# Kernel optimization log

Hardware: AMD Instinct MI355X
Metric: run time of the kernel (lower is better)

Reference implementation:

```python
import jax, jax.numpy as jnp
import numpy as np

BLOCK = 32          # MXFP block size (OCP microscaling)
EMAX_FP4 = 2.0      # max exponent of FP4 E2M1 (max value 6.0 = 1.5 * 2^2)
FP4_MAX = 6.0       # saturation value of E2M1
E8M0_MIN, E8M0_MAX = -127.0, 127.0


def _quant_dequant_mxfp(t, block_dim):
    """Fake-quantize tensor t to MXFP4 (E2M1 elements, shared E8M0 scale per
    block of 32 along block_dim), then dequantize back to float."""
    t = jnp.moveaxis(t, block_dim, -1)
    shape = t.shape
    nb = shape[-1] // BLOCK
    tb = t.reshape(shape[:-1] + (nb, BLOCK))

    # shared power-of-two scale from block absmax: scale = 2^(floor(log2 amax) - emax)
    amax = jnp.max(jnp.abs(tb), axis=-1, keepdims=True)
    safe_amax = jnp.where(amax > 0, amax, 1.0)
    shared_exp = jnp.floor(jnp.log2(safe_amax)) - EMAX_FP4
    scale = jnp.exp2(jnp.clip(shared_exp, E8M0_MIN, E8M0_MAX))

    v = tb / scale
    sign = jnp.sign(v)
    a = jnp.clip(jnp.abs(v), 0.0, FP4_MAX)  # saturate to E2M1 max
    # E2M1 quantization step: 0.5 for |v|<2 (incl. subnormals), 1 for [2,4), 2 for [4,6]
    e = jnp.clip(jnp.floor(jnp.log2(jnp.maximum(a, 2.0 ** -10))), 0.0, EMAX_FP4)
    step = jnp.exp2(e - 1.0)
    q = jnp.round(a / step) * step

    deq = (sign * q * scale).reshape(shape)
    return jnp.moveaxis(deq, -1, block_dim)


def setup_inputs() -> dict:
    key = jax.random.key(0)
    kx, kw, kb = jax.random.split(key, 3)
    x = jax.random.normal(kx, (64, 4096), dtype=jnp.float32)
    weight = jax.random.normal(kw, (11008, 4096), dtype=jnp.float32) * 0.02
    bias = jax.random.normal(kb, (11008,), dtype=jnp.float32) * 0.02
    return {"x": x, "weight": weight, "bias": bias}


def reference(x, weight, bias):
    # layer_type = 'XqWqBq': MXFP4 quant-dequant on x (last dim), w (in_features
    # dim, block_dim=1) and b (dim 0), fused with the linear GEMM.
    x_dq = _quant_dequant_mxfp(x, block_dim=-1)        # [T, Din]
    w_dq = _quant_dequant_mxfp(weight, block_dim=1)    # [Dout, Din]
    b_dq = _quant_dequant_mxfp(bias, block_dim=0)      # [Dout]
    return jnp.einsum('ti,oi->to', x_dq, w_dq) + b_dq  # [T, Dout]
```

## Files before the change

### kernel.cpp

```cpp
#include <hip/hip_runtime.h>
#include <hip/hip_bf16.h>

#define DIN   4096
#define DOUT  11008
#define TM    64
#define KSPLIT 4
#define KCHUNK (DIN / KSPLIT)

typedef __attribute__((ext_vector_type(8))) short  bf16x8;
typedef __attribute__((ext_vector_type(4))) float  f32x4;

__device__ inline void mx_block_scale(float amax, float& scale, float& inv_scale) {
    float safe = amax > 0.0f ? amax : 1.0f;
    int e = (int)((__float_as_uint(safe) >> 23) & 255) - 127;
    int se = e - 2;
    if (se < -127) se = -127;
    scale     = ldexpf(1.0f, se);
    inv_scale = ldexpf(1.0f, -se);
}

__device__ inline float mx_qd(float v, float scale, float inv_scale) {
    float a = fabsf(v) * inv_scale;
    a = fminf(a, 6.0f);
    float step, rstep;
    if (a < 2.0f)      { step = 0.5f; rstep = 2.0f; }
    else if (a < 4.0f) { step = 1.0f; rstep = 1.0f; }
    else               { step = 2.0f; rstep = 0.5f; }
    float q = rintf(a * rstep) * step;
    return copysignf(q * scale, v);
}

__device__ inline unsigned short f32_to_bf16_bits(float f) {
    return (unsigned short)(__float_as_uint(f) >> 16);
}

__global__ __launch_bounds__(256) void quant_x_kernel(const float* __restrict__ x,
                                                      unsigned short* __restrict__ x_dq) {
    int gid = blockIdx.x * 256 + threadIdx.x;
    const float4 v = *(const float4*)(x + (size_t)gid * 4);
    float am = fmaxf(fmaxf(fabsf(v.x), fabsf(v.y)), fmaxf(fabsf(v.z), fabsf(v.w)));
    am = fmaxf(am, __shfl_xor(am, 1));
    am = fmaxf(am, __shfl_xor(am, 2));
    am = fmaxf(am, __shfl_xor(am, 4));
    float scale, inv;
    mx_block_scale(am, scale, inv);
    ushort4 q;
    q.x = f32_to_bf16_bits(mx_qd(v.x, scale, inv));
    q.y = f32_to_bf16_bits(mx_qd(v.y, scale, inv));
    q.z = f32_to_bf16_bits(mx_qd(v.z, scale, inv));
    q.w = f32_to_bf16_bits(mx_qd(v.w, scale, inv));
    *(ushort4*)(x_dq + (size_t)gid * 4) = q;
}

__global__ __launch_bounds__(64) void init_out_kernel(const float* __restrict__ bias,
                                                      float* __restrict__ out) {
    int n = blockIdx.x * 64 + threadIdx.x;
    float v = bias[n];
    float am = fabsf(v);
    am = fmaxf(am, __shfl_xor(am, 1));
    am = fmaxf(am, __shfl_xor(am, 2));
    am = fmaxf(am, __shfl_xor(am, 4));
    am = fmaxf(am, __shfl_xor(am, 8));
    am = fmaxf(am, __shfl_xor(am, 16));
    float scale, inv;
    mx_block_scale(am, scale, inv);
    float b = mx_qd(v, scale, inv);
    for (int t = 0; t < TM; ++t)
        out[(size_t)t * DOUT + n] = b;
}

__global__ __launch_bounds__(256) void gemm_kernel(const unsigned short* __restrict__ x_dq,
                                                   const float* __restrict__ wgt,
                                                   float* __restrict__ out) {
    __shared__ unsigned short x_lds[TM * 32];
    __shared__ unsigned short w_lds[32 * 32];

    const int t     = threadIdx.x;
    const int lane  = t & 63;
    const int wid   = t >> 6;
    const int n0    = blockIdx.x * 32;
    const int kbase = blockIdx.y * KCHUNK;

    const int wrow = t >> 3;
    const int wcol = (t & 7) * 4;
    const int xrow = t >> 2;
    const int xcol = (t & 3) * 8;

    const float*          wptr = wgt + (size_t)(n0 + wrow) * DIN + kbase + wcol;
    const unsigned short* xptr = x_dq + (size_t)xrow * DIN + kbase + xcol;

    const int a_off  = (wid * 16 + (lane & 15)) * 32 + (lane >> 4) * 8;
    const int b_off0 = (lane & 15) * 32 + (lane >> 4) * 8;
    const int b_off1 = b_off0 + 16 * 32;

    f32x4 acc0 = {0.f, 0.f, 0.f, 0.f};
    f32x4 acc1 = {0.f, 0.f, 0.f, 0.f};

    for (int kk = 0; kk < KCHUNK; kk += 32) {
        const float4 wv = *(const float4*)(wptr + kk);
        float am = fmaxf(fmaxf(fabsf(wv.x), fabsf(wv.y)), fmaxf(fabsf(wv.z), fabsf(wv.w)));
        am = fmaxf(am, __shfl_xor(am, 1));
        am = fmaxf(am, __shfl_xor(am, 2));
        am = fmaxf(am, __shfl_xor(am, 4));
        float scale, inv;
        mx_block_scale(am, scale, inv);
        ushort4 qw;
        qw.x = f32_to_bf16_bits(mx_qd(wv.x, scale, inv));
        qw.y = f32_to_bf16_bits(mx_qd(wv.y, scale, inv));
        qw.z = f32_to_bf16_bits(mx_qd(wv.z, scale, inv));
        qw.w = f32_to_bf16_bits(mx_qd(wv.w, scale, inv));
        *(ushort4*)(w_lds + wrow * 32 + wcol) = qw;

        *(uint4*)(x_lds + xrow * 32 + xcol) = *(const uint4*)(xptr + kk);

        __syncthreads();

        bf16x8 af = *(const bf16x8*)(x_lds + a_off);
        bf16x8 b0 = *(const bf16x8*)(w_lds + b_off0);
        bf16x8 b1 = *(const bf16x8*)(w_lds + b_off1);
        acc0 = __builtin_amdgcn_mfma_f32_16x16x32_bf16(af, b0, acc0, 0, 0, 0);
        acc1 = __builtin_amdgcn_mfma_f32_16x16x32_bf16(af, b1, acc1, 0, 0, 0);

        __syncthreads();
    }

    const int m = wid * 16 + ((lane >> 4) << 2);
    const int n = n0 + (lane & 15);
    for (int r = 0; r < 4; ++r) {
        atomicAdd(&out[(size_t)(m + r) * DOUT + n],      acc0[r]);
        atomicAdd(&out[(size_t)(m + r) * DOUT + n + 16], acc1[r]);
    }
}

extern "C" void kernel_launch(void* const* d_in, const int* in_sizes, int n_in,
                              void* d_out, int out_size, void* d_ws, size_t ws_size,
                              hipStream_t stream) {
    const float* x    = (const float*)d_in[0];
    const float* wgt  = (const float*)d_in[1];
    const float* bias = (const float*)d_in[2];
    float* out = (float*)d_out;
    unsigned short* x_dq = (unsigned short*)d_ws;

    quant_x_kernel<<<256, 256, 0, stream>>>(x, x_dq);
    init_out_kernel<<<172, 64, 0, stream>>>(bias, out);
    gemm_kernel<<<dim3(DOUT / 32, KSPLIT), 256, 0, stream>>>(x_dq, wgt, out);
}
```

Measured before the change: 279.2 us.

## Restructure GEMM to LDS-free per-wave tiles with split-K partials and reduce kernel

Each wave now owns a 16-column output slice and one of eight K-chunks, loading weights directly into registers in MFMA operand layout with a one-step register prefetch. Block absmax is reduced via cross-lane shuffles, removing shared-memory staging and both barriers per iteration. Atomic accumulation is replaced by writing per-split partial sums to workspace, followed by a separate reduce kernel that adds the quantized bias. This trades extra partial-sum traffic and a kernel launch for removing syncs and atomics.

```diff
diff --git a/kernel.cpp b/kernel.cpp
--- a/kernel.cpp
+++ b/kernel.cpp
@@ -1,18 +1,19 @@
 #include <hip/hip_runtime.h>
 #include <hip/hip_bf16.h>
 
-#define DIN   4096
-#define DOUT  11008
-#define TM    64
-#define KSPLIT 4
+#define DIN    4096
+#define DOUT   11008
+#define TM     64
+#define KSPLIT 8
 #define KCHUNK (DIN / KSPLIT)
+#define NCHUNKS (DOUT / 16)
 
 typedef __attribute__((ext_vector_type(8))) short  bf16x8;
 typedef __attribute__((ext_vector_type(4))) float  f32x4;
 
 __device__ inline void mx_block_scale(float amax, float& scale, float& inv_scale) {
     float safe = amax > 0.0f ? amax : 1.0f;
-    int e = (int)((__float_as_uint(safe) >> 23) & 255) - 127;
+    int e  = (int)((__float_as_uint(safe) >> 23) & 255) - 127;
     int se = e - 2;
     if (se < -127) se = -127;
     scale     = ldexpf(1.0f, se);
@@ -22,16 +23,14 @@
 __device__ inline float mx_qd(float v, float scale, float inv_scale) {
     float a = fabsf(v) * inv_scale;
     a = fminf(a, 6.0f);
-    float step, rstep;
-    if (a < 2.0f)      { step = 0.5f; rstep = 2.0f; }
-    else if (a < 4.0f) { step = 1.0f; rstep = 1.0f; }
-    else               { step = 2.0f; rstep = 0.5f; }
+    float step  = (a < 2.0f) ? 0.5f : (a < 4.0f) ? 1.0f : 2.0f;
+    float rstep = (a < 2.0f) ? 2.0f : (a < 4.0f) ? 1.0f : 0.5f;
     float q = rintf(a * rstep) * step;
     return copysignf(q * scale, v);
 }
 
-__device__ inline unsigned short f32_to_bf16_bits(float f) {
-    return (unsigned short)(__float_as_uint(f) >> 16);
+__device__ inline short bf16_trunc(float f) {
+    return (short)(__float_as_uint(f) >> 16);
 }
 
 __global__ __launch_bounds__(256) void quant_x_kernel(const float* __restrict__ x,
@@ -45,16 +44,90 @@
     float scale, inv;
     mx_block_scale(am, scale, inv);
     ushort4 q;
-    q.x = f32_to_bf16_bits(mx_qd(v.x, scale, inv));
-    q.y = f32_to_bf16_bits(mx_qd(v.y, scale, inv));
-    q.z = f32_to_bf16_bits(mx_qd(v.z, scale, inv));
-    q.w = f32_to_bf16_bits(mx_qd(v.w, scale, inv));
+    q.x = (unsigned short)bf16_trunc(mx_qd(v.x, scale, inv));
+    q.y = (unsigned short)bf16_trunc(mx_qd(v.y, scale, inv));
+    q.z = (unsigned short)bf16_trunc(mx_qd(v.z, scale, inv));
+    q.w = (unsigned short)bf16_trunc(mx_qd(v.w, scale, inv));
     *(ushort4*)(x_dq + (size_t)gid * 4) = q;
 }
 
-__global__ __launch_bounds__(64) void init_out_kernel(const float* __restrict__ bias,
-                                                      float* __restrict__ out) {
-    int n = blockIdx.x * 64 + threadIdx.x;
+__global__ __launch_bounds__(256) void gemm_kernel(const unsigned short* __restrict__ x_dq,
+                                                   const float* __restrict__ wgt,
+                                                   float* __restrict__ partial) {
+    const int lane  = threadIdx.x & 63;
+    const int wid   = threadIdx.x >> 6;
+    const int w     = blockIdx.x * 4 + wid;
+    const int nch   = w % NCHUNKS;
+    const int split = w / NCHUNKS;
+    const int nlo   = lane & 15;
+    const int kq    = lane >> 4;
+    const int kbase = split * KCHUNK + kq * 8;
+
+    const float*          wp = wgt  + (size_t)(nch * 16 + nlo) * DIN + kbase;
+    const unsigned short* xp = x_dq + (size_t)nlo * DIN + kbase;
+
+    f32x4 acc0 = {0.f,0.f,0.f,0.f};
+    f32x4 acc1 = {0.f,0.f,0.f,0.f};
+    f32x4 acc2 = {0.f,0.f,0.f,0.f};
+    f32x4 acc3 = {0.f,0.f,0.f,0.f};
+
+    float4 w0 = *(const float4*)(wp);
+    float4 w1 = *(const float4*)(wp + 4);
+
+    for (int kk = 0; kk < KCHUNK; kk += 32) {
+        float4 c0 = w0, c1 = w1;
+        if (kk + 32 < KCHUNK) {
+            w0 = *(const float4*)(wp + kk + 32);
+            w1 = *(const float4*)(wp + kk + 36);
+        }
+        bf16x8 a0 = *(const bf16x8*)(xp + kk);
+        bf16x8 a1 = *(const bf16x8*)(xp + 16 * DIN + kk);
+        bf16x8 a2 = *(const bf16x8*)(xp + 32 * DIN + kk);
+        bf16x8 a3 = *(const bf16x8*)(xp + 48 * DIN + kk);
+
+        float am = fmaxf(fmaxf(fmaxf(fabsf(c0.x), fabsf(c0.y)), fmaxf(fabsf(c0.z), fabsf(c0.w))),
+                         fmaxf(fmaxf(fabsf(c1.x), fabsf(c1.y)), fmaxf(fabsf(c1.z), fabsf(c1.w))));
+        am = fmaxf(am, __shfl_xor(am, 16));
+        am = fmaxf(am, __shfl_xor(am, 32));
+        float scale, inv;
+        mx_block_scale(am, scale, inv);
+
+        bf16x8 bf;
+        bf[0] = bf16_trunc(mx_qd(c0.x, scale, inv));
+        bf[1] = bf16_trunc(mx_qd(c0.y, scale, inv));
+        bf[2] = bf16_trunc(mx_qd(c0.z, scale, inv));
+        bf[3] = bf16_trunc(mx_qd(c0.w, scale, inv));
+        bf[4] = bf16_trunc(mx_qd(c1.x, scale, inv));
+        bf[5] = bf16_trunc(mx_qd(c1.y, scale, inv));
+        bf[6] = bf16_trunc(mx_qd(c1.z, scale, inv));
+        bf[7] = bf16_trunc(mx_qd(c1.w, scale, inv));
+
+        acc0 = __builtin_amdgcn_mfma_f32_16x16x32_bf16(a0, bf, acc0, 0, 0, 0);
+        acc1 = __builtin_amdgcn_mfma_f32_16x16x32_bf16(a1, bf, acc1, 0, 0, 0);
+        acc2 = __builtin_amdgcn_mfma_f32_16x16x32_bf16(a2, bf, acc2, 0, 0, 0);
+        acc3 = __builtin_amdgcn_mfma_f32_16x16x32_bf16(a3, bf, acc3, 0, 0, 0);
+    }
+
+    float* pp = partial + (size_t)split * (TM * DOUT) + (size_t)(nch * 16 + nlo);
+    const int mrow = kq * 4;
+    #pragma unroll
+    for (int r = 0; r < 4; ++r) {
+        pp[(size_t)(mrow + r) * DOUT]      = acc0[r];
+        pp[(size_t)(16 + mrow + r) * DOUT] = acc1[r];
+        pp[(size_t)(32 + mrow + r) * DOUT] = acc2[r];
+        pp[(size_t)(48 + mrow + r) * DOUT] = acc3[r];
+    }
+}
+
+__global__ __launch_bounds__(256) void reduce_bias_kernel(const float* __restrict__ partial,
+                                                          const float* __restrict__ bias,
+                                                          float* __restrict__ out) {
+    int gid = blockIdx.x * 256 + threadIdx.x;
+    float s = 0.f;
+    #pragma unroll
+    for (int i = 0; i < KSPLIT; ++i)
+        s += partial[(size_t)i * (TM * DOUT) + gid];
+    int n = gid % DOUT;
     float v = bias[n];
     float am = fabsf(v);
     am = fmaxf(am, __shfl_xor(am, 1));
@@ -64,72 +137,7 @@
     am = fmaxf(am, __shfl_xor(am, 16));
     float scale, inv;
     mx_block_scale(am, scale, inv);
-    float b = mx_qd(v, scale, inv);
-    for (int t = 0; t < TM; ++t)
-        out[(size_t)t * DOUT + n] = b;
-}
-
-__global__ __launch_bounds__(256) void gemm_kernel(const unsigned short* __restrict__ x_dq,
-                                                   const float* __restrict__ wgt,
-                                                   float* __restrict__ out) {
-    __shared__ unsigned short x_lds[TM * 32];
-    __shared__ unsigned short w_lds[32 * 32];
-
-    const int t     = threadIdx.x;
-    const int lane  = t & 63;
-    const int wid   = t >> 6;
-    const int n0    = blockIdx.x * 32;
-    const int kbase = blockIdx.y * KCHUNK;
-
-    const int wrow = t >> 3;
-    const int wcol = (t & 7) * 4;
-    const int xrow = t >> 2;
-    const int xcol = (t & 3) * 8;
-
-    const float*          wptr = wgt + (size_t)(n0 + wrow) * DIN + kbase + wcol;
-    const unsigned short* xptr = x_dq + (size_t)xrow * DIN + kbase + xcol;
-
-    const int a_off  = (wid * 16 + (lane & 15)) * 32 + (lane >> 4) * 8;
-    const int b_off0 = (lane & 15) * 32 + (lane >> 4) * 8;
-    const int b_off1 = b_off0 + 16 * 32;
-
-    f32x4 acc0 = {0.f, 0.f, 0.f, 0.f};
-    f32x4 acc1 = {0.f, 0.f, 0.f, 0.f};
-
-    for (int kk = 0; kk < KCHUNK; kk += 32) {
-        const float4 wv = *(const float4*)(wptr + kk);
-        float am = fmaxf(fmaxf(fabsf(wv.x), fabsf(wv.y)), fmaxf(fabsf(wv.z), fabsf(wv.w)));
-        am = fmaxf(am, __shfl_xor(am, 1));
-        am = fmaxf(am, __shfl_xor(am, 2));
-        am = fmaxf(am, __shfl_xor(am, 4));
-        float scale, inv;
-        mx_block_scale(am, scale, inv);
-        ushort4 qw;
-        qw.x = f32_to_bf16_bits(mx_qd(wv.x, scale, inv));
-        qw.y = f32_to_bf16_bits(mx_qd(wv.y, scale, inv));
-        qw.z = f32_to_bf16_bits(mx_qd(wv.z, scale, inv));
-        qw.w = f32_to_bf16_bits(mx_qd(wv.w, scale, inv));
-        *(ushort4*)(w_lds + wrow * 32 + wcol) = qw;
-
-        *(uint4*)(x_lds + xrow * 32 + xcol) = *(const uint4*)(xptr + kk);
-
-        __syncthreads();
-
-        bf16x8 af = *(const bf16x8*)(x_lds + a_off);
-        bf16x8 b0 = *(const bf16x8*)(w_lds + b_off0);
-        bf16x8 b1 = *(const bf16x8*)(w_lds + b_off1);
-        acc0 = __builtin_amdgcn_mfma_f32_16x16x32_bf16(af, b0, acc0, 0, 0, 0);
-        acc1 = __builtin_amdgcn_mfma_f32_16x16x32_bf16(af, b1, acc1, 0, 0, 0);
-
-        __syncthreads();
-    }
-
-    const int m = wid * 16 + ((lane >> 4) << 2);
-    const int n = n0 + (lane & 15);
-    for (int r = 0; r < 4; ++r) {
-        atomicAdd(&out[(size_t)(m + r) * DOUT + n],      acc0[r]);
-        atomicAdd(&out[(size_t)(m + r) * DOUT + n + 16], acc1[r]);
-    }
+    out[gid] = s + mx_qd(v, scale, inv);
 }
 
 extern "C" void kernel_launch(void* const* d_in, const int* in_sizes, int n_in,
@@ -139,9 +147,11 @@
     const float* wgt  = (const float*)d_in[1];
     const float* bias = (const float*)d_in[2];
     float* out = (float*)d_out;
-    unsigned short* x_dq = (unsigned short*)d_ws;
+
+    unsigned short* x_dq    = (unsigned short*)d_ws;
+    float*          partial = (float*)((char*)d_ws + 512 * 1024);
 
     quant_x_kernel<<<256, 256, 0, stream>>>(x, x_dq);
-    init_out_kernel<<<172, 64, 0, stream>>>(bias, out);
-    gemm_kernel<<<dim3(DOUT / 32, KSPLIT), 256, 0, stream>>>(x_dq, wgt, out);
+    gemm_kernel<<<NCHUNKS * KSPLIT / 4, 256, 0, stream>>>(x_dq, wgt, partial);
+    reduce_bias_kernel<<<TM * DOUT / 256, 256, 0, stream>>>(partial, bias, out);
 }
```

Result: slower. 290.5 us (+4.1%).
